# Kernel tuning notes

Hardware: AMD Instinct MI355X
Metric: run time of the kernel (lower is better)

## Reference

```python
import jax, jax.numpy as jnp
import numpy as np
from jax.scipy.special import ndtri

BLOCK_SIZE = 32
NF5_OFFSET = 0.9677083  # QLoRA-style tail quantile offset


def _nf5_table():
    # 32-level NormalFloat-5 table: 16 negative levels, zero, 15 positive levels,
    # taken from standard-normal quantiles and normalized so endpoints hit -1 / +1.
    neg = ndtri(jnp.linspace(1.0 - NF5_OFFSET, 0.5, 17))[:-1]   # 16 negative quantiles
    pos = ndtri(jnp.linspace(0.5, NF5_OFFSET, 16))[1:]          # 15 positive quantiles
    neg = neg / (-neg[0])
    pos = pos / pos[-1]
    return jnp.concatenate([neg, jnp.zeros((1,)), pos]).astype(jnp.float32)


def nf5_quantize(x, block_size, table, boundaries):
    # Block-wise NF5 quantization with power-of-2 scales along the last dim.
    shp = x.shape
    xb = x.reshape(-1, block_size)                               # [nblocks, B]
    amax = jnp.max(jnp.abs(xb), axis=1, keepdims=True)
    scale = jnp.exp2(jnp.ceil(jnp.log2(jnp.maximum(amax, 1e-12))))  # power-of-2 scale
    n = xb / scale                                               # normalized to [-1, 1]
    idx = jnp.searchsorted(boundaries, n)                        # nearest-level index
    q = table[idx] * scale                                       # fused dequant
    return q.reshape(shp)


def setup_inputs() -> dict:
    key = jax.random.key(0)
    k1, k2, k3 = jax.random.split(key, 3)
    B, S, Din, Dout = 8, 4096, 1024, 1024
    x = jax.random.normal(k1, (B, S, Din), dtype=jnp.float32)
    # kaiming_uniform_(a=sqrt(5)) -> U(-b, b) with b = sqrt(6/((1+5)*fan_in)) = 1/sqrt(fan_in)
    bound_w = 1.0 / np.sqrt(Din)
    weight = jax.random.uniform(k2, (Dout, Din), minval=-bound_w, maxval=bound_w, dtype=jnp.float32)
    bias = jax.random.uniform(k3, (Dout,), minval=-bound_w, maxval=bound_w, dtype=jnp.float32)
    return {"x": x, "weight": weight, "bias": bias}


def reference(x, weight, bias):
    table = _nf5_table()
    boundaries = (table[:-1] + table[1:]) * 0.5
    qw = nf5_quantize(weight, BLOCK_SIZE, table, boundaries)   # quantize weight along in_features
    qx = nf5_quantize(x, BLOCK_SIZE, table, boundaries)        # quantize_input=True
    # y[b,s,o] = sum_k qx[b,s,k] * qw[o,k] + bias[o]
    y = jnp.einsum('bsk,ok->bso', qx, qw) + bias
    return y
```

## Files before the change

### kernel.cpp

```cpp
#include <hip/hip_runtime.h>
#include <hip/hip_bf16.h>

typedef __attribute__((ext_vector_type(8))) short short8;
typedef __attribute__((ext_vector_type(4))) float f32x4;

struct alignas(16) US8 { unsigned short s[8]; };

__device__ double ndtri_d(double p) {
    const double a1 = -3.969683028665376e+01, a2 = 2.209460984245205e+02,
                 a3 = -2.759285104469687e+02, a4 = 1.383577518672690e+02,
                 a5 = -3.066479806614716e+01, a6 = 2.506628277459239e+00;
    const double b1 = -5.447609879822406e+01, b2 = 1.615858368580409e+02,
                 b3 = -1.556989798598866e+02, b4 = 6.680131188771972e+01,
                 b5 = -1.328068155288572e+01;
    const double c1 = -7.784894002430293e-03, c2 = -3.223964580411365e-01,
                 c3 = -2.400758277161838e+00, c4 = -2.549732539343734e+00,
                 c5 = 4.374664141464968e+00,  c6 = 2.938163982698783e+00;
    const double d1 = 7.784695709041462e-03, d2 = 3.224671290700398e-01,
                 d3 = 2.445134137142996e+00, d4 = 3.754408661907416e+00;
    const double plow = 0.02425, phigh = 1.0 - 0.02425;
    double x;
    if (p < plow) {
        double q = sqrt(-2.0 * log(p));
        x = (((((c1*q+c2)*q+c3)*q+c4)*q+c5)*q+c6) / ((((d1*q+d2)*q+d3)*q+d4)*q+1.0);
    } else if (p <= phigh) {
        double q = p - 0.5, r = q * q;
        x = (((((a1*r+a2)*r+a3)*r+a4)*r+a5)*r+a6)*q / (((((b1*r+b2)*r+b3)*r+b4)*r+b5)*r+1.0);
    } else {
        double q = sqrt(-2.0 * log(1.0 - p));
        x = -(((((c1*q+c2)*q+c3)*q+c4)*q+c5)*q+c6) / ((((d1*q+d2)*q+d3)*q+d4)*q+1.0);
    }
    #pragma unroll
    for (int it = 0; it < 2; ++it) {
        double e = 0.5 * erfc(-x * 0.70710678118654752440) - p;
        double u = e * 2.50662827463100050242 * exp(0.5 * x * x);
        x = x - u / (1.0 + 0.5 * x * u);
    }
    return x;
}

__global__ void build_table_k(float* __restrict__ table, float* __restrict__ bounds,
                              unsigned char* __restrict__ lut) {
    __shared__ float sT[32], sBd[32];
    const int i = threadIdx.x;
    const double OFF = 0.9677083;
    double v;
    if (i == 16) {
        v = 0.0;
    } else if (i < 16) {
        const double a = 1.0 - OFF;
        double p = a + (0.5 - a) * ((double)i / 16.0);
        v = ndtri_d(p) / (-ndtri_d(a));
    } else {
        int j = i - 16;
        double p = 0.5 + (OFF - 0.5) * ((double)j / 15.0);
        v = ndtri_d(p) / ndtri_d(OFF);
    }
    float tv = (float)v;
    sT[i] = tv;
    table[i] = tv;
    __syncthreads();
    float bd;
    if (i < 31) bd = 0.5f * (sT[i] + sT[i + 1]);
    else        bd = __builtin_inff();
    sBd[i] = bd;
    bounds[i] = bd;
    __syncthreads();
    for (int j = i; j < 256; j += 32) {
        float nj = (float)j * (1.0f / 128.0f) - 1.0f - 0x1p-20f;
        int c = 0;
        #pragma unroll
        for (int k = 0; k < 31; ++k) c += (sBd[k] < nj) ? 1 : 0;
        lut[j] = (unsigned char)c;
    }
}

__device__ __forceinline__ unsigned short q_one(float n, float scale,
                                                const float* sT, const float* sBnd,
                                                const unsigned char* sLut) {
    float u = fmaf(n, 0.5f, 0.5f);
    int b = (int)(u * 256.0f);
    b = min(b, 255);
    int base = sLut[b];
    int idx = base + ((sBnd[base] < n) ? 1 : 0);
    float q = sT[idx] * scale;
    __hip_bfloat16 h = __float2bfloat16(q);
    return *reinterpret_cast<unsigned short*>(&h);
}

__global__ __launch_bounds__(256) void quantize_k(const float4* __restrict__ x,
                                                  US8* __restrict__ qx, int nblk_x, int n8x,
                                                  const float4* __restrict__ wgt,
                                                  US8* __restrict__ qw, int n8w,
                                                  const float* __restrict__ table,
                                                  const float* __restrict__ bounds,
                                                  const unsigned char* __restrict__ lut) {
    __shared__ float sT[32], sBnd[32];
    __shared__ unsigned char sLut[256];
    const int tid = threadIdx.x;
    if (tid < 32) { sT[tid] = table[tid]; sBnd[tid] = bounds[tid]; }
    sLut[tid] = lut[tid];
    __syncthreads();
    const float4* in; US8* out; int t, n8;
    if ((int)blockIdx.x < nblk_x) { in = x;   out = qx; t = blockIdx.x * 256 + tid;            n8 = n8x; }
    else                          { in = wgt; out = qw; t = (blockIdx.x - nblk_x) * 256 + tid; n8 = n8w; }
    if (t >= n8) return;
    float4 v0 = in[2 * t];
    float4 v1 = in[2 * t + 1];
    float am = fmaxf(fmaxf(fmaxf(fabsf(v0.x), fabsf(v0.y)), fmaxf(fabsf(v0.z), fabsf(v0.w))),
                     fmaxf(fmaxf(fabsf(v1.x), fabsf(v1.y)), fmaxf(fabsf(v1.z), fabsf(v1.w))));
    am = fmaxf(am, __shfl_xor(am, 1));
    am = fmaxf(am, __shfl_xor(am, 2));
    am = fmaxf(am, 1e-12f);
    int e;
    float m = frexpf(am, &e);
    int se = (m == 0.5f) ? (e - 1) : e;
    float scale = ldexpf(1.0f, se);
    float inv   = ldexpf(1.0f, -se);
    US8 o;
    o.s[0] = q_one(v0.x * inv, scale, sT, sBnd, sLut);
    o.s[1] = q_one(v0.y * inv, scale, sT, sBnd, sLut);
    o.s[2] = q_one(v0.z * inv, scale, sT, sBnd, sLut);
    o.s[3] = q_one(v0.w * inv, scale, sT, sBnd, sLut);
    o.s[4] = q_one(v1.x * inv, scale, sT, sBnd, sLut);
    o.s[5] = q_one(v1.y * inv, scale, sT, sBnd, sLut);
    o.s[6] = q_one(v1.z * inv, scale, sT, sBnd, sLut);
    o.s[7] = q_one(v1.w * inv, scale, sT, sBnd, sLut);
    out[t] = o;
}

__device__ __forceinline__ void gload_lds16(const unsigned short* g, unsigned short* s) {
    __builtin_amdgcn_global_load_lds(
        (const __attribute__((address_space(1))) unsigned int*)g,
        (__attribute__((address_space(3))) unsigned int*)s, 16, 0, 0);
}

#define STAGE2(G0, C0, G1, C1, SM, T1)                                       \
    { const int sl_ = (T1) & 1;                                              \
      gload_lds16((G0) + (size_t)(T1) * 64, &SM[sl_][(C0) * 512]);           \
      gload_lds16((G1) + (size_t)(T1) * 64, &SM[sl_][(C1) * 512]); }

#define READ_A(DST, MQ, SLOT)                                                \
    _Pragma("unroll")                                                        \
    for (int ks = 0; ks < 2; ++ks) {                                         \
        const int k8_ = ks * 4 + quad;                                       \
        _Pragma("unroll")                                                    \
        for (int i = 0; i < 4; ++i) {                                        \
            const int ra = wm + (MQ) * 64 + i * 16 + rsel;                   \
            DST[ks][i] = *(const short8*)&sA[SLOT][                          \
                ((ra >> 3) * 64 + (ra & 7) * 8 + ((k8_ ^ ra) & 7)) * 8];     \
        }                                                                    \
    }

#define READ_B(DST, NQ, SLOT)                                                \
    _Pragma("unroll")                                                        \
    for (int ks = 0; ks < 2; ++ks) {                                         \
        const int k8_ = ks * 4 + quad;                                       \
        _Pragma("unroll")                                                    \
        for (int j = 0; j < 2; ++j) {                                        \
            const int rb = wn + (NQ) * 32 + j * 16 + rsel;                   \
            DST[ks][j] = *(const short8*)&sB[SLOT][                          \
                ((rb >> 3) * 64 + (rb & 7) * 8 + ((k8_ ^ rb) & 7)) * 8];     \
        }                                                                    \
    }

#define MFMA16(AF, BF, IOFF, JOFF)                                           \
    __builtin_amdgcn_s_setprio(1);                                           \
    _Pragma("unroll")                                                        \
    for (int ks = 0; ks < 2; ++ks)                                           \
        _Pragma("unroll")                                                    \
        for (int i = 0; i < 4; ++i)                                          \
            _Pragma("unroll")                                                \
            for (int j = 0; j < 2; ++j)                                      \
                acc[(IOFF) + i][(JOFF) + j] =                                \
                    __builtin_amdgcn_mfma_f32_16x16x32_bf16(                 \
                        AF[ks][i], BF[ks][j],                                \
                        acc[(IOFF) + i][(JOFF) + j], 0, 0, 0);               \
    __builtin_amdgcn_s_setprio(0);

#define VMW(N) asm volatile("s_waitcnt vmcnt(" #N ")" ::: "memory")

__global__ __launch_bounds__(512, 1) void gemm_bt_k(const unsigned short* __restrict__ A,
                                                    const unsigned short* __restrict__ B,
                                                    const float* __restrict__ bias,
                                                    float* __restrict__ C,
                                                    int M, int N, int K) {
    __shared__ unsigned short sA[2][256 * 64];
    __shared__ unsigned short sB[2][256 * 64];
    const int t = threadIdx.x;
    const int w = t >> 6, l = t & 63;

    const int nB = N >> 8, mB = M >> 8;
    int m_idx, n_idx;
    {
        const unsigned int lin = blockIdx.x;
        const unsigned int nwg = (unsigned int)(nB * mB);
        unsigned int gid = lin;
        if ((nwg & 7u) == 0u) {
            const unsigned int per = nwg >> 3;
            gid = (lin & 7u) * per + (lin >> 3);
        }
        n_idx = (int)(gid % (unsigned int)nB);
        m_idx = (int)(gid / (unsigned int)nB);
    }
    const int m_blk = m_idx << 8, n_blk = n_idx << 8;
    const int wm = (w >> 2) * 128;
    const int wn = (w & 3) * 64;
    const int rsel = l & 15, quad = l >> 4;

    const int st_row = l >> 3;
    const int st_oct = (l & 7) ^ st_row;
    const int ja0 = 2 * w, ja1 = 2 * w + 1;
    const int cA1_0 = (ja0 < 8) ? ja0 : ja0 + 8;
    const int cA1_1 = (ja1 < 8) ? ja1 : ja1 + 8;
    const int cA2_0 = cA1_0 + 8, cA2_1 = cA1_1 + 8;
    const int cB1_0 = (ja0 & 3) + (ja0 >> 2) * 8;
    const int cB1_1 = (ja1 & 3) + (ja1 >> 2) * 8;
    const int cB2_0 = cB1_0 + 4, cB2_1 = cB1_1 + 4;

    const unsigned short* gA1_0 = A + (size_t)(m_blk + cA1_0 * 8 + st_row) * K + st_oct * 8;
    const unsigned short* gA1_1 = A + (size_t)(m_blk + cA1_1 * 8 + st_row) * K + st_oct * 8;
    const unsigned short* gA2_0 = A + (size_t)(m_blk + cA2_0 * 8 + st_row) * K + st_oct * 8;
    const unsigned short* gA2_1 = A + (size_t)(m_blk + cA2_1 * 8 + st_row) * K + st_oct * 8;
    const unsigned short* gB1_0 = B + (size_t)(n_blk + cB1_0 * 8 + st_row) * K + st_oct * 8;
    const unsigned short* gB1_1 = B + (size_t)(n_blk + cB1_1 * 8 + st_row) * K + st_oct * 8;
    const unsigned short* gB2_0 = B + (size_t)(n_blk + cB2_0 * 8 + st_row) * K + st_oct * 8;
    const unsigned short* gB2_1 = B + (size_t)(n_blk + cB2_1 * 8 + st_row) * K + st_oct * 8;

    f32x4 acc[8][4];
    #pragma unroll
    for (int i = 0; i < 8; ++i)
        #pragma unroll
        for (int j = 0; j < 4; ++j)
            acc[i][j] = (f32x4){0.f, 0.f, 0.f, 0.f};

    STAGE2(gA1_0, cA1_0, gA1_1, cA1_1, sA, 0);
    STAGE2(gB1_0, cB1_0, gB1_1, cB1_1, sB, 0);
    STAGE2(gB2_0, cB2_0, gB2_1, cB2_1, sB, 0);
    STAGE2(gA2_0, cA2_0, gA2_1, cA2_1, sA, 0);

    const int nt = K >> 6;
    for (int tt = 0; tt < nt - 1; ++tt) {
        const int sl = tt & 1;
        short8 aF[2][4], b0F[2][2], b1F[2][2];
        VMW(4);
        __builtin_amdgcn_s_barrier();
        READ_A(aF, 0, sl);
        READ_B(b0F, 0, sl);
        STAGE2(gA1_0, cA1_0, gA1_1, cA1_1, sA, tt + 1);
        MFMA16(aF, b0F, 0, 0);
        VMW(4);
        __builtin_amdgcn_s_barrier();
        READ_B(b1F, 1, sl);
        STAGE2(gB1_0, cB1_0, gB1_1, cB1_1, sB, tt + 1);
        MFMA16(aF, b1F, 0, 2);
        VMW(4);
        __builtin_amdgcn_s_barrier();
        READ_A(aF, 1, sl);
        STAGE2(gB2_0, cB2_0, gB2_1, cB2_1, sB, tt + 1);
        MFMA16(aF, b1F, 4, 2);
        STAGE2(gA2_0, cA2_0, gA2_1, cA2_1, sA, tt + 1);
        MFMA16(aF, b0F, 4, 0);
    }
    {
        const int sl = (nt - 1) & 1;
        short8 aF[2][4], b0F[2][2], b1F[2][2];
        VMW(4);
        __builtin_amdgcn_s_barrier();
        READ_A(aF, 0, sl);
        READ_B(b0F, 0, sl);
        MFMA16(aF, b0F, 0, 0);
        VMW(2);
        __builtin_amdgcn_s_barrier();
        READ_B(b1F, 1, sl);
        MFMA16(aF, b1F, 0, 2);
        VMW(0);
        __builtin_amdgcn_s_barrier();
        READ_A(aF, 1, sl);
        MFMA16(aF, b1F, 4, 2);
        MFMA16(aF, b0F, 4, 0);
    }

    float bv[4];
    #pragma unroll
    for (int jj = 0; jj < 4; ++jj) bv[jj] = bias[n_blk + wn + jj * 16 + rsel];
    #pragma unroll
    for (int ii = 0; ii < 8; ++ii) {
        const int rbase = m_blk + wm + (ii >> 2) * 64 + (ii & 3) * 16 + quad * 4;
        #pragma unroll
        for (int r = 0; r < 4; ++r) {
            float* cp = C + (size_t)(rbase + r) * N + n_blk + wn + rsel;
            #pragma unroll
            for (int jj = 0; jj < 4; ++jj)
                cp[jj * 16] = acc[ii][jj][r] + bv[jj];
        }
    }
}

extern "C" void kernel_launch(void* const* d_in, const int* in_sizes, int n_in,
                              void* d_out, int out_size, void* d_ws, size_t ws_size,
                              hipStream_t stream) {
    const float* x    = (const float*)d_in[0];
    const float* wgt  = (const float*)d_in[1];
    const float* bias = (const float*)d_in[2];
    float* out = (float*)d_out;

    const int x_size = in_sizes[0];
    const int w_size = in_sizes[1];
    const int N = in_sizes[2];
    const int K = w_size / N;
    const int M = x_size / K;

    char* ws = (char*)d_ws;
    unsigned short* qx = (unsigned short*)ws;
    unsigned short* qw = (unsigned short*)(ws + (size_t)M * K * sizeof(unsigned short));
    float* table  = (float*)(ws + (size_t)M * K * 2 + (size_t)N * K * 2);
    float* bounds = table + 32;
    unsigned char* lut = (unsigned char*)(bounds + 32);

    build_table_k<<<1, 32, 0, stream>>>(table, bounds, lut);

    const int n8x = x_size / 8, n8w = w_size / 8;
    const int nblk_x = (n8x + 255) / 256, nblk_w = (n8w + 255) / 256;
    quantize_k<<<nblk_x + nblk_w, 256, 0, stream>>>(
        (const float4*)x, (US8*)qx, nblk_x, n8x,
        (const float4*)wgt, (US8*)qw, n8w, table, bounds, lut);

    const int grid = (M / 256) * (N / 256);
    gemm_bt_k<<<grid, 512, 0, stream>>>(qx, qw, bias, out, M, N, K);
}
```

Before: 304.9 us.

## Restructure GEMM main loop into k-split phases with full-width B fragments

Reorganizes the LDS fragment reads and MFMA phases so each phase uses one k-substep with all four N-subtiles instead of both k-substeps with two N-subtiles. This changes the interleaving of global-to-LDS staging with compute, reduces barriers per tile from three to two, and adds sched_barrier fences to pin the ordering of reads, loads and MFMAs. The aim is better overlap of LDS reads and async copies with matrix math. The new ordering must keep the vmcnt waits and slot reuse correct, and the larger set of live fragment registers could raise register pressure.

```diff
diff --git a/kernel.cpp b/kernel.cpp
--- a/kernel.cpp
+++ b/kernel.cpp
@@ -140,45 +140,41 @@
       gload_lds16((G0) + (size_t)(T1) * 64, &SM[sl_][(C0) * 512]);           \
       gload_lds16((G1) + (size_t)(T1) * 64, &SM[sl_][(C1) * 512]); }
 
-#define READ_A(DST, MQ, SLOT)                                                \
-    _Pragma("unroll")                                                        \
-    for (int ks = 0; ks < 2; ++ks) {                                         \
-        const int k8_ = ks * 4 + quad;                                       \
+#define READ_A1(DST, MQ, KS, SLOT)                                           \
+    {                                                                        \
+        const int k8_ = (KS) * 4 + quad;                                     \
         _Pragma("unroll")                                                    \
         for (int i = 0; i < 4; ++i) {                                        \
             const int ra = wm + (MQ) * 64 + i * 16 + rsel;                   \
-            DST[ks][i] = *(const short8*)&sA[SLOT][                          \
+            DST[i] = *(const short8*)&sA[SLOT][                              \
                 ((ra >> 3) * 64 + (ra & 7) * 8 + ((k8_ ^ ra) & 7)) * 8];     \
         }                                                                    \
     }
 
-#define READ_B(DST, NQ, SLOT)                                                \
-    _Pragma("unroll")                                                        \
-    for (int ks = 0; ks < 2; ++ks) {                                         \
-        const int k8_ = ks * 4 + quad;                                       \
+#define READ_B1(DST, KS, SLOT)                                               \
+    {                                                                        \
+        const int k8_ = (KS) * 4 + quad;                                     \
         _Pragma("unroll")                                                    \
-        for (int j = 0; j < 2; ++j) {                                        \
-            const int rb = wn + (NQ) * 32 + j * 16 + rsel;                   \
-            DST[ks][j] = *(const short8*)&sB[SLOT][                          \
+        for (int j = 0; j < 4; ++j) {                                        \
+            const int rb = wn + j * 16 + rsel;                               \
+            DST[j] = *(const short8*)&sB[SLOT][                              \
                 ((rb >> 3) * 64 + (rb & 7) * 8 + ((k8_ ^ rb) & 7)) * 8];     \
         }                                                                    \
     }
 
-#define MFMA16(AF, BF, IOFF, JOFF)                                           \
+#define MFMA_PH(AB, BB, MQ)                                                  \
     __builtin_amdgcn_s_setprio(1);                                           \
     _Pragma("unroll")                                                        \
-    for (int ks = 0; ks < 2; ++ks)                                           \
+    for (int i = 0; i < 4; ++i)                                              \
         _Pragma("unroll")                                                    \
-        for (int i = 0; i < 4; ++i)                                          \
-            _Pragma("unroll")                                                \
-            for (int j = 0; j < 2; ++j)                                      \
-                acc[(IOFF) + i][(JOFF) + j] =                                \
-                    __builtin_amdgcn_mfma_f32_16x16x32_bf16(                 \
-                        AF[ks][i], BF[ks][j],                                \
-                        acc[(IOFF) + i][(JOFF) + j], 0, 0, 0);               \
+        for (int j = 0; j < 4; ++j)                                          \
+            acc[(MQ) * 4 + i][j] =                                           \
+                __builtin_amdgcn_mfma_f32_16x16x32_bf16(                     \
+                    AB[i], BB[j], acc[(MQ) * 4 + i][j], 0, 0, 0);            \
     __builtin_amdgcn_s_setprio(0);
 
 #define VMW(N) asm volatile("s_waitcnt vmcnt(" #N ")" ::: "memory")
+#define SCHED_FENCE() __builtin_amdgcn_sched_barrier(0)
 
 __global__ __launch_bounds__(512, 1) void gemm_bt_k(const unsigned short* __restrict__ A,
                                                     const unsigned short* __restrict__ B,
@@ -234,51 +230,58 @@
         for (int j = 0; j < 4; ++j)
             acc[i][j] = (f32x4){0.f, 0.f, 0.f, 0.f};
 
-    STAGE2(gA1_0, cA1_0, gA1_1, cA1_1, sA, 0);
     STAGE2(gB1_0, cB1_0, gB1_1, cB1_1, sB, 0);
     STAGE2(gB2_0, cB2_0, gB2_1, cB2_1, sB, 0);
+    STAGE2(gA1_0, cA1_0, gA1_1, cA1_1, sA, 0);
     STAGE2(gA2_0, cA2_0, gA2_1, cA2_1, sA, 0);
+
+    short8 Ab0[4], Ab1[4], Bb0[4], Bb1[4];
 
     const int nt = K >> 6;
     for (int tt = 0; tt < nt - 1; ++tt) {
         const int sl = tt & 1;
-        short8 aF[2][4], b0F[2][2], b1F[2][2];
-        VMW(4);
+        VMW(2);
         __builtin_amdgcn_s_barrier();
-        READ_A(aF, 0, sl);
-        READ_B(b0F, 0, sl);
+        READ_A1(Ab0, 0, 0, sl);
+        READ_B1(Bb0, 0, sl);
+        READ_A1(Ab1, 0, 1, sl);
+        READ_B1(Bb1, 1, sl);
+        STAGE2(gB1_0, cB1_0, gB1_1, cB1_1, sB, tt + 1);
+        SCHED_FENCE();
+        MFMA_PH(Ab0, Bb0, 0);
+        VMW(2);
+        __builtin_amdgcn_s_barrier();
+        READ_A1(Ab0, 1, 1, sl);
+        STAGE2(gB2_0, cB2_0, gB2_1, cB2_1, sB, tt + 1);
+        SCHED_FENCE();
+        MFMA_PH(Ab1, Bb1, 0);
+        READ_A1(Ab1, 1, 0, sl);
         STAGE2(gA1_0, cA1_0, gA1_1, cA1_1, sA, tt + 1);
-        MFMA16(aF, b0F, 0, 0);
-        VMW(4);
-        __builtin_amdgcn_s_barrier();
-        READ_B(b1F, 1, sl);
-        STAGE2(gB1_0, cB1_0, gB1_1, cB1_1, sB, tt + 1);
-        MFMA16(aF, b1F, 0, 2);
-        VMW(4);
-        __builtin_amdgcn_s_barrier();
-        READ_A(aF, 1, sl);
-        STAGE2(gB2_0, cB2_0, gB2_1, cB2_1, sB, tt + 1);
-        MFMA16(aF, b1F, 4, 2);
+        SCHED_FENCE();
+        MFMA_PH(Ab0, Bb1, 1);
         STAGE2(gA2_0, cA2_0, gA2_1, cA2_1, sA, tt + 1);
-        MFMA16(aF, b0F, 4, 0);
+        SCHED_FENCE();
+        MFMA_PH(Ab1, Bb0, 1);
     }
     {
         const int sl = (nt - 1) & 1;
-        short8 aF[2][4], b0F[2][2], b1F[2][2];
-        VMW(4);
-        __builtin_amdgcn_s_barrier();
-        READ_A(aF, 0, sl);
-        READ_B(b0F, 0, sl);
-        MFMA16(aF, b0F, 0, 0);
         VMW(2);
         __builtin_amdgcn_s_barrier();
-        READ_B(b1F, 1, sl);
-        MFMA16(aF, b1F, 0, 2);
+        READ_A1(Ab0, 0, 0, sl);
+        READ_B1(Bb0, 0, sl);
+        READ_A1(Ab1, 0, 1, sl);
+        READ_B1(Bb1, 1, sl);
+        SCHED_FENCE();
+        MFMA_PH(Ab0, Bb0, 0);
         VMW(0);
         __builtin_amdgcn_s_barrier();
-        READ_A(aF, 1, sl);
-        MFMA16(aF, b1F, 4, 2);
-        MFMA16(aF, b0F, 4, 0);
+        READ_A1(Ab0, 1, 1, sl);
+        SCHED_FENCE();
+        MFMA_PH(Ab1, Bb1, 0);
+        READ_A1(Ab1, 1, 0, sl);
+        SCHED_FENCE();
+        MFMA_PH(Ab0, Bb1, 1);
+        MFMA_PH(Ab1, Bb0, 1);
     }
 
     float bv[4];
```

After: 296.0 us. 2.9% less time.
